# Kernel tuning notes

Measured on AMD Instinct MI355X. Metric: run time of the kernel, lower is better.

The kernel has to match this reference:

```python
import jax, jax.numpy as jnp
import numpy as np

IMG = 800          # image size (square)
STRIDE = 4         # feature-map stride
S = 14             # rcnn_crop_size
C = 256            # crop_channels
N = 512            # number of rpn proposals
NUM_CLASSES = 81   # COCO (incl. background at index 0)
HID = 1024
NMS_TH = 0.5
SCORE_TH = 0.05


def setup_inputs() -> dict:
    key = jax.random.key(0)
    ks = jax.random.split(key, 8)
    features = jax.random.normal(ks[0], (1, C, IMG // STRIDE, IMG // STRIDE), jnp.float32)
    # valid proposal boxes (x0, y0, x1, y1) in image coordinates
    u = jax.random.uniform(ks[1], (N, 4), jnp.float32)
    x0 = u[:, 0] * (IMG - 64.0)
    y0 = u[:, 1] * (IMG - 64.0)
    bw = 16.0 + u[:, 2] * 240.0
    bh = 16.0 + u[:, 3] * 240.0
    proposals = jnp.stack([x0, y0, jnp.minimum(x0 + bw, IMG - 1.0), jnp.minimum(y0 + bh, IMG - 1.0)], axis=1)
    d1 = C * S * S  # 50176
    w1 = jax.random.normal(ks[2], (d1, HID), jnp.float32) * (1.0 / np.sqrt(d1))
    b1 = jnp.zeros((HID,), jnp.float32)
    w2 = jax.random.normal(ks[3], (HID, HID), jnp.float32) * (1.0 / np.sqrt(HID))
    b2 = jnp.zeros((HID,), jnp.float32)
    w_cls = jax.random.normal(ks[4], (HID, NUM_CLASSES), jnp.float32) * (1.0 / np.sqrt(HID))
    b_cls = jnp.zeros((NUM_CLASSES,), jnp.float32)
    w_reg = jax.random.normal(ks[5], (HID, NUM_CLASSES * 4), jnp.float32) * (1.0 / np.sqrt(HID))
    b_reg = jnp.zeros((NUM_CLASSES * 4,), jnp.float32)
    return dict(features=features, proposals=proposals, w1=w1, b1=b1, w2=w2, b2=b2,
                w_cls=w_cls, b_cls=b_cls, w_reg=w_reg, b_reg=b_reg)


def roi_align(feat, boxes):
    """feat: [C,H,W]; boxes: [N,4] image coords -> crops [N,C,S,S] via bilinear sampling (1 sample per bin)."""
    _, H, W = feat.shape
    b = boxes / STRIDE
    t = (jnp.arange(S, dtype=feat.dtype) + 0.5) / S                # [S] bin centers
    xs = b[:, 0:1] + (b[:, 2:3] - b[:, 0:1]) * t                   # [N,S]
    ys = b[:, 1:2] + (b[:, 3:4] - b[:, 1:2]) * t                   # [N,S]
    xx = jnp.broadcast_to(xs[:, None, :], (boxes.shape[0], S, S))  # [N,S,S]
    yy = jnp.broadcast_to(ys[:, :, None], (boxes.shape[0], S, S))
    x0f = jnp.floor(xx); y0f = jnp.floor(yy)
    fx = xx - x0f; fy = yy - y0f
    x0i = jnp.clip(x0f.astype(jnp.int32), 0, W - 1); x1i = jnp.clip(x0i + 1, 0, W - 1)
    y0i = jnp.clip(y0f.astype(jnp.int32), 0, H - 1); y1i = jnp.clip(y0i + 1, 0, H - 1)
    # gathers -> [C,N,S,S]
    v = (((1 - fx) * (1 - fy))[None] * feat[:, y0i, x0i]
         + (fx * (1 - fy))[None] * feat[:, y0i, x1i]
         + ((1 - fx) * fy)[None] * feat[:, y1i, x0i]
         + (fx * fy)[None] * feat[:, y1i, x1i])
    return v.transpose(1, 0, 2, 3)  # [N,C,S,S]


def decode_boxes(rois, d):
    w = rois[:, 2] - rois[:, 0]; h = rois[:, 3] - rois[:, 1]
    cx = rois[:, 0] + 0.5 * w; cy = rois[:, 1] + 0.5 * h
    px = cx + d[:, 0] * w; py = cy + d[:, 1] * h
    pw = w * jnp.exp(jnp.clip(d[:, 2], -4.0, 4.0))
    ph = h * jnp.exp(jnp.clip(d[:, 3], -4.0, 4.0))
    b = jnp.stack([px - 0.5 * pw, py - 0.5 * ph, px + 0.5 * pw, py + 0.5 * ph], axis=1)
    return jnp.clip(b, 0.0, IMG - 1.0)


def iou_matrix(b):
    area = jnp.maximum(b[:, 2] - b[:, 0], 0.0) * jnp.maximum(b[:, 3] - b[:, 1], 0.0)
    ix0 = jnp.maximum(b[:, None, 0], b[None, :, 0])
    iy0 = jnp.maximum(b[:, None, 1], b[None, :, 1])
    ix1 = jnp.minimum(b[:, None, 2], b[None, :, 2])
    iy1 = jnp.minimum(b[:, None, 3], b[None, :, 3])
    inter = jnp.maximum(ix1 - ix0, 0.0) * jnp.maximum(iy1 - iy0, 0.0)
    return inter / (area[:, None] + area[None, :] - inter + 1e-6)


def reference(features, proposals, w1, b1, w2, b2, w_cls, b_cls, w_reg, b_reg):
    # 1) RoIAlign crop
    crops = roi_align(features[0], proposals)              # [N,C,S,S]
    # 2) RCNN head
    x = crops.reshape(N, -1)
    x = jax.nn.relu(x @ w1 + b1)
    x = jax.nn.relu(x @ w2 + b2)
    logits = x @ w_cls + b_cls                             # [N,81]
    deltas = (x @ w_reg + b_reg).reshape(N, NUM_CLASSES, 4)
    # 3) NMS post-processing
    probs = jax.nn.softmax(logits, axis=-1)
    fg = probs[:, 1:]                                      # exclude background
    labels = jnp.argmax(fg, axis=-1) + 1                   # [N]
    scores = jnp.max(fg, axis=-1)                          # [N]
    d = deltas[jnp.arange(N), labels]                      # per-ROI delta of predicted class
    boxes = decode_boxes(proposals, d)
    order = jnp.argsort(-scores)
    bs = boxes[order]; ss = scores[order]; ls = labels[order]
    valid = ss > SCORE_TH
    M = iou_matrix(bs)                                     # [N,N]
    idx = jnp.arange(N)
    def body(i, keep):
        alive = keep[i] & valid[i]
        supp = (M[i] > NMS_TH) & (idx > i) & alive
        return keep & (~supp)
    keep = jax.lax.fori_loop(0, N, body, valid)
    keepf = jax.lax.stop_gradient(keep.astype(bs.dtype))
    final = jnp.concatenate([bs, ss[:, None]], axis=1) * keepf[:, None]   # [N,5]
    return final, ls.astype(jnp.int32), keep
```

## Files before the change

kernel.cpp:

```cpp
#include <hip/hip_runtime.h>
#include <cstdint>

#define F_H 200
#define F_W 200
#define D1  50176
#define NBOX 512
#define NHID 1024

typedef _Float16 f16;
typedef _Float16 half8 __attribute__((ext_vector_type(8)));
typedef _Float16 half4v __attribute__((ext_vector_type(4)));
typedef _Float16 half2v __attribute__((ext_vector_type(2)));
typedef float    f32x4 __attribute__((ext_vector_type(4)));

__device__ __forceinline__ void gload16(const void* g, void* l) {
  __builtin_amdgcn_global_load_lds((const __attribute__((address_space(1))) void*)g,
                                   (__attribute__((address_space(3))) void*)l,
                                   16, 0, 0);
}

__device__ __forceinline__ half2v pkrtz(float a, float b) {
  return __builtin_bit_cast(half2v, __builtin_amdgcn_cvt_pkrtz(a, b));
}

__device__ __forceinline__ void splitf16(float v, f16& h, f16& l) {
  f16 hh = (f16)v;
  float hf = (float)hh;
  if (fabsf(hf) < 6.1035156e-5f) hf = 0.f;
  h = (f16)hh;
  if (fabsf(hf) < 6.1035156e-5f) h = (f16)0.f;
  l = (f16)((v - hf) * 2048.f);
}

__global__ __launch_bounds__(256) void k_roi(const float* __restrict__ feat,
                                             const float* __restrict__ prop,
                                             f16* __restrict__ xhi, f16* __restrict__ xlo) {
  uint32_t idx = blockIdx.x * 256u + threadIdx.x;
  uint32_t n = idx / 25088u;
  uint32_t rem = idx % 25088u;
  uint32_t c = rem / 98u;
  uint32_t r2 = rem % 98u;
  uint32_t i = r2 / 7u;
  uint32_t jp = r2 % 7u;
  float b0 = prop[n * 4 + 0] * 0.25f, b1 = prop[n * 4 + 1] * 0.25f;
  float b2 = prop[n * 4 + 2] * 0.25f, b3 = prop[n * 4 + 3] * 0.25f;
  float ty = ((float)i + 0.5f) * (1.0f / 14.0f);
  float yy = b1 + (b3 - b1) * ty;
  float y0f = floorf(yy);
  float fy = yy - y0f;
  int y0 = (int)y0f; y0 = y0 < 0 ? 0 : (y0 > F_H - 1 ? F_H - 1 : y0);
  int y1 = y0 + 1 > F_H - 1 ? F_H - 1 : y0 + 1;
  const float* fr0 = feat + (size_t)c * (F_H * F_W) + (size_t)y0 * F_W;
  const float* fr1 = feat + (size_t)c * (F_H * F_W) + (size_t)y1 * F_W;
  f16 hs[2], ls[2];
#pragma unroll
  for (int e = 0; e < 2; ++e) {
    uint32_t j = jp * 2u + (uint32_t)e;
    float tx = ((float)j + 0.5f) * (1.0f / 14.0f);
    float xx = b0 + (b2 - b0) * tx;
    float x0f = floorf(xx);
    float fx = xx - x0f;
    int x0 = (int)x0f; x0 = x0 < 0 ? 0 : (x0 > F_W - 1 ? F_W - 1 : x0);
    int x1 = x0 + 1 > F_W - 1 ? F_W - 1 : x0 + 1;
    float v00 = fr0[x0], v01 = fr0[x1], v10 = fr1[x0], v11 = fr1[x1];
    float v = (1.f - fx) * (1.f - fy) * v00 + fx * (1.f - fy) * v01 +
              (1.f - fx) * fy * v10 + fx * fy * v11;
    splitf16(v, hs[e], ls[e]);
  }
  uint32_t base = n * 50176u + c * 196u + i * 14u + jp * 2u;
  half2v hv; hv[0] = hs[0]; hv[1] = hs[1];
  half2v lv; lv[0] = ls[0]; lv[1] = ls[1];
  *(half2v*)(xhi + base) = hv;
  *(half2v*)(xlo + base) = lv;
}

__global__ __launch_bounds__(256) void k_tsplit(const float* __restrict__ W,
                                                f16* __restrict__ hiT, f16* __restrict__ loT,
                                                int Kdim, int Ndim) {
  __shared__ f16 lh[64 * 72];
  __shared__ f16 ll[64 * 72];
  int t = threadIdx.x;
  int k0 = blockIdx.x * 64, n0 = blockIdx.y * 64;
  int r = t >> 2, cq = t & 3;
  const float* src = W + (size_t)(k0 + r) * Ndim + n0 + cq * 16;
  f16 hv[16], lv[16];
#pragma unroll
  for (int e = 0; e < 4; ++e) {
    f32x4 v = *(const f32x4*)(src + e * 4);
#pragma unroll
    for (int x = 0; x < 4; ++x) splitf16(v[x], hv[e * 4 + x], lv[e * 4 + x]);
  }
#pragma unroll
  for (int j = 0; j < 16; ++j) {
    int n_l = cq * 16 + j;
    lh[n_l * 72 + r] = hv[j];
    ll[n_l * 72 + r] = lv[j];
  }
  __syncthreads();
  f16* oh = hiT + (size_t)(n0 + r) * Kdim + k0 + cq * 16;
  f16* ol = loT + (size_t)(n0 + r) * Kdim + k0 + cq * 16;
  *(half8*)(oh)     = *(const half8*)(&lh[r * 72 + cq * 16]);
  *(half8*)(oh + 8) = *(const half8*)(&lh[r * 72 + cq * 16 + 8]);
  *(half8*)(ol)     = *(const half8*)(&ll[r * 72 + cq * 16]);
  *(half8*)(ol + 8) = *(const half8*)(&ll[r * 72 + cq * 16 + 8]);
}

__global__ __launch_bounds__(256) void k_packT(const float* __restrict__ wc_, const float* __restrict__ bc,
                                               const float* __restrict__ wr_, const float* __restrict__ br,
                                               f16* __restrict__ whT_hi, f16* __restrict__ whT_lo,
                                               float* __restrict__ bh) {
  uint32_t idx = blockIdx.x * 256u + threadIdx.x;
  if (idx < 512u * 1024u) {
    uint32_t n = idx >> 10, k = idx & 1023u;
    float v = 0.f;
    if (n < 81u) v = wc_[k * 81u + n];
    else if (n < 405u) v = wr_[k * 324u + (n - 81u)];
    f16 h, l; splitf16(v, h, l);
    whT_hi[idx] = h; whT_lo[idx] = l;
  } else if (idx < 512u * 1024u + 512u) {
    uint32_t n = idx - 512u * 1024u;
    float v = 0.f;
    if (n < 81u) v = bc[n];
    else if (n < 405u) v = br[n - 81u];
    bh[n] = v;
  }
}

__global__ __launch_bounds__(512, 2) void k_gemm2(
    const f16* __restrict__ Ahi, const f16* __restrict__ Alo,
    const f16* __restrict__ Bhi, const f16* __restrict__ Blo,
    float* __restrict__ Cp, int K, int N, int Kc, int nMt, int nNt)
{
  __shared__ char sm[131072];
  const int t = threadIdx.x;
  const int lane = t & 63;
  const int wid = t >> 6;
  const int wr = wid >> 2;
  const int wc = wid & 3;
  const int rl = lane & 15;
  const int lq = lane >> 4;

  int bid = blockIdx.x;
  int low = bid & 7, qq = bid >> 3;
  int nt = qq % nNt;
  int chi = qq / nNt;
  int c = chi * 8 + low;
  int ks = c / nMt;
  int mt = c % nMt;
  const int brow = mt * 256;
  const int nbase = nt * 256;
  const int k0 = ks * Kc;
  const int nk = Kc >> 5;

  uint32_t aoffg[2], aldso[2];
#pragma unroll
  for (int i = 0; i < 2; ++i) {
    uint32_t idx = (uint32_t)t + 512u * i;
    uint32_t q2 = idx >> 2, s = idx & 3;
    uint32_t qh = q2 >> 6;
    uint32_t grh = (qh == 1u) ? 2u : (qh == 2u) ? 1u : qh;
    uint32_t gr = grh * 64u + (q2 & 63u);
    aoffg[i] = (uint32_t)(brow + gr) * (uint32_t)K + (s ^ ((q2 >> 1) & 3u)) * 8u;
    aldso[i] = idx * 16u;
  }
  uint32_t boffg[2], bldso[2];
#pragma unroll
  for (int i = 0; i < 2; ++i) {
    uint32_t idx = (uint32_t)t + 512u * i;
    uint32_t rB = idx >> 2, s = idx & 3;
    boffg[i] = (uint32_t)(nbase + rB) * (uint32_t)K + (s ^ ((rB >> 1) & 3u)) * 8u;
    bldso[i] = idx * 16u;
  }

  const uint32_t swzk = (uint32_t)(lq ^ ((rl >> 1) & 3)) * 16u;
  const uint32_t a_off_lane = (uint32_t)(rl * 64) + swzk;
  const uint32_t b_off_lane = (uint32_t)((wc * 16 + rl) * 64) + swzk;

  f32x4 zero4 = {0.f, 0.f, 0.f, 0.f};
  f32x4 acc[8][4];
#pragma unroll
  for (int m = 0; m < 8; ++m)
#pragma unroll
    for (int n = 0; n < 4; ++n) acc[m][n] = zero4;

#define PH0STAGE(LB, KB) do { \
    gload16(Bhi + boffg[0] + (KB), (LB) + 32768 + bldso[0]); \
    gload16(Blo + boffg[0] + (KB), (LB) + 49152 + bldso[0]); \
    gload16(Bhi + boffg[1] + (KB), (LB) + 32768 + bldso[1]); \
    gload16(Blo + boffg[1] + (KB), (LB) + 49152 + bldso[1]); \
    gload16(Ahi + aoffg[0] + (KB), (LB) + aldso[0]); \
    gload16(Alo + aoffg[0] + (KB), (LB) + 16384 + aldso[0]); \
  } while (0)

#define PH1STAGE(LB, KB) do { \
    gload16(Ahi + aoffg[1] + (KB), (LB) + aldso[1]); \
    gload16(Alo + aoffg[1] + (KB), (LB) + 16384 + aldso[1]); \
  } while (0)

#define COMPUTE_PHASE(P) do { \
    half8 bh2[4], bl2[4]; \
    _Pragma("unroll") \
    for (int nf = 0; nf < 4; ++nf) { \
      bh2[nf] = *(const half8*)(lb + 32768 + nf * 4096 + b_off_lane); \
      bl2[nf] = *(const half8*)(lb + 49152 + nf * 4096 + b_off_lane); \
    } \
    __builtin_amdgcn_s_setprio(1); \
    _Pragma("unroll") \
    for (int mm = 0; mm < 4; ++mm) { \
      const char* ab = lb + (P) * 8192 + wr * 4096 + mm * 1024 + a_off_lane; \
      half8 ah = *(const half8*)(ab); \
      half8 al = *(const half8*)(ab + 16384); \
      _Pragma("unroll") \
      for (int nf = 0; nf < 4; ++nf) { \
        acc[(P)*4+mm][nf] = __builtin_amdgcn_mfma_f32_16x16x32_f16(ah, bh2[nf], acc[(P)*4+mm][nf], 0, 0, 0); \
        f32x4 tt = __builtin_amdgcn_mfma_f32_16x16x32_f16(ah, bl2[nf], zero4, 0, 0, 0); \
        tt = __builtin_amdgcn_mfma_f32_16x16x32_f16(al, bh2[nf], tt, 0, 0, 0); \
        acc[(P)*4+mm][nf] += tt * 4.8828125e-4f; \
      } \
    } \
    __builtin_amdgcn_s_setprio(0); \
  } while (0)

  PH0STAGE(sm, (uint32_t)k0);
  PH1STAGE(sm, (uint32_t)k0);

  int cur = 0;
  for (int kt = 0; kt < nk; ++kt) {
    int ktn = (kt + 1 < nk) ? kt + 1 : kt;
    uint32_t kbn = (uint32_t)(k0 + ktn * 32);
    const char* lb = sm + cur * 65536;
    char* lbn = sm + (cur ^ 1) * 65536;

    asm volatile("s_waitcnt vmcnt(2)" ::: "memory");
    __builtin_amdgcn_s_barrier();
    __builtin_amdgcn_sched_barrier(0);
    PH0STAGE(lbn, kbn);
    COMPUTE_PHASE(0);

    asm volatile("s_waitcnt vmcnt(6)" ::: "memory");
    __builtin_amdgcn_s_barrier();
    __builtin_amdgcn_sched_barrier(0);
    PH1STAGE(lbn, kbn);
    COMPUTE_PHASE(1);

    cur ^= 1;
  }

  float* Cs = Cp + (size_t)ks * ((size_t)512 * (uint32_t)N);
#pragma unroll
  for (int m = 0; m < 8; ++m) {
    int rg = brow + wr * 128 + m * 16 + lq * 4;
#pragma unroll
    for (int nf = 0; nf < 4; ++nf) {
      int cg = nbase + nf * 64 + wc * 16 + rl;
#pragma unroll
      for (int rr = 0; rr < 4; ++rr)
        Cs[(size_t)(rg + rr) * (uint32_t)N + cg] = acc[m][nf][rr];
    }
  }
#undef PH0STAGE
#undef PH1STAGE
}

__global__ __launch_bounds__(512, 2) void k_gemm3(
    const f16* __restrict__ Ahi, const f16* __restrict__ Alo,
    const float* __restrict__ B, float* __restrict__ Cp,
    int K, int N, int Kc, int nMt, int nNt)
{
  __shared__ char sm[131072];
  const int t = threadIdx.x;
  const int lane = t & 63;
  const int wid = t >> 6;
  const int wr = wid >> 2;
  const int wc = wid & 3;
  const int rl = lane & 15;
  const int lq = lane >> 4;

  int bid = blockIdx.x;
  int low = bid & 7, qq = bid >> 3;
  int nt = qq % nNt;
  int chi = qq / nNt;
  int c = chi * 8 + low;
  int ks = c / nMt;
  int mt = c % nMt;
  const int brow = mt * 256;
  const int nbase = nt * 256;
  const int k0 = ks * Kc;
  const int nk = Kc >> 5;

  uint32_t aoffg[2], aldso[2];
#pragma unroll
  for (int i = 0; i < 2; ++i) {
    uint32_t idx = (uint32_t)t + 512u * i;
    uint32_t q2 = idx >> 2, s = idx & 3;
    uint32_t qh = q2 >> 6;
    uint32_t grh = (qh == 1u) ? 2u : (qh == 2u) ? 1u : qh;
    uint32_t gr = grh * 64u + (q2 & 63u);
    aoffg[i] = (uint32_t)(brow + gr) * (uint32_t)K + (s ^ ((q2 >> 1) & 3u)) * 8u;
    aldso[i] = idx * 16u;
  }

  const uint32_t nrow = (uint32_t)t & 255u;
  const uint32_t kh = (uint32_t)t >> 8;
  const float* bsrc0 = B + (size_t)((uint32_t)k0 + kh * 16u) * (uint32_t)N + (uint32_t)nbase + nrow;
  const uint32_t bswz = (nrow >> 1) & 3u;
  const uint32_t wb0 = nrow * 64u + (((kh * 2u)      ^ bswz) << 4);
  const uint32_t wb1 = nrow * 64u + (((kh * 2u + 1u) ^ bswz) << 4);

  const uint32_t swzk = (uint32_t)(lq ^ ((rl >> 1) & 3)) * 16u;
  const uint32_t a_off_lane = (uint32_t)(rl * 64) + swzk;
  const uint32_t b_off_lane = (uint32_t)((wc * 16 + rl) * 64) + swzk;

  f32x4 zero4 = {0.f, 0.f, 0.f, 0.f};
  f32x4 acc[8][4];
#pragma unroll
  for (int m = 0; m < 8; ++m)
#pragma unroll
    for (int n = 0; n < 4; ++n) acc[m][n] = zero4;

  float bx[16], by[16];

#define LOADB(ARR, KT) do { \
    const float* bp = bsrc0 + (size_t)((uint32_t)(KT) * 32u) * (uint32_t)N; \
    _Pragma("unroll") \
    for (int j = 0; j < 16; ++j) ARR[j] = bp[(size_t)j * (uint32_t)N]; \
  } while (0)

#define WRITEB(LB, ARR) do { \
    half8 h0, l0, h1, l1; \
    _Pragma("unroll") \
    for (int j = 0; j < 16; j += 2) { \
      float v0 = ARR[j], v1 = ARR[j + 1]; \
      half2v hp = pkrtz(v0, v1); \
      f16 e0 = (fabsf(v0) >= 6.1035156e-5f) ? hp[0] : (f16)0; \
      f16 e1 = (fabsf(v1) >= 6.1035156e-5f) ? hp[1] : (f16)0; \
      half2v lp = pkrtz((v0 - (float)e0) * 2048.f, (v1 - (float)e1) * 2048.f); \
      if (j < 8) { h0[j] = e0; h0[j + 1] = e1; l0[j] = lp[0]; l0[j + 1] = lp[1]; } \
      else { h1[j - 8] = e0; h1[j - 7] = e1; l1[j - 8] = lp[0]; l1[j - 7] = lp[1]; } \
    } \
    *(half8*)((LB) + 32768 + wb0) = h0; \
    *(half8*)((LB) + 49152 + wb0) = l0; \
    *(half8*)((LB) + 32768 + wb1) = h1; \
    *(half8*)((LB) + 49152 + wb1) = l1; \
  } while (0)

#define STAGE_A4(LB, KB) do { \
    gload16(Ahi + aoffg[0] + (KB), (LB) + aldso[0]); \
    gload16(Alo + aoffg[0] + (KB), (LB) + 16384 + aldso[0]); \
    gload16(Ahi + aoffg[1] + (KB), (LB) + aldso[1]); \
    gload16(Alo + aoffg[1] + (KB), (LB) + 16384 + aldso[1]); \
  } while (0)

#define ITER(KT, IN, OUT) do { \
    int kA = ((KT) + 1 < nk) ? (KT) + 1 : nk - 1; \
    int kB = ((KT) + 2 < nk) ? (KT) + 2 : nk - 1; \
    const char* lb = sm + cur * 65536; \
    char* lbn = sm + (cur ^ 1) * 65536; \
    STAGE_A4(lbn, (uint32_t)(k0 + kA * 32));   \
    LOADB(OUT, kB);                            \
    COMPUTE_PHASE(0); \
    asm volatile("s_waitcnt vmcnt(20)" ::: "memory");   \
    __builtin_amdgcn_sched_barrier(0); \
    WRITEB(lbn, IN); \
    COMPUTE_PHASE(1); \
    asm volatile("s_waitcnt vmcnt(16) lgkmcnt(0)" ::: "memory");   \
    __builtin_amdgcn_sched_barrier(0); \
    __builtin_amdgcn_s_barrier(); \
    cur ^= 1; \
  } while (0)

  LOADB(bx, 0);
  STAGE_A4(sm, (uint32_t)k0);
  asm volatile("s_waitcnt vmcnt(4)" ::: "memory");
  __builtin_amdgcn_sched_barrier(0);
  WRITEB(sm, bx);
  LOADB(by, (nk > 1) ? 1 : 0);
  asm volatile("s_waitcnt vmcnt(16) lgkmcnt(0)" ::: "memory");
  __builtin_amdgcn_sched_barrier(0);
  __builtin_amdgcn_s_barrier();

  int cur = 0;
  int kt = 0;
  for (; kt + 1 < nk; kt += 2) {
    ITER(kt, by, bx);
    ITER(kt + 1, bx, by);
  }
  if (kt < nk) ITER(kt, by, bx);

  float* Cs = Cp + (size_t)ks * ((size_t)512 * (uint32_t)N);
#pragma unroll
  for (int m = 0; m < 8; ++m) {
    int rg = brow + wr * 128 + m * 16 + lq * 4;
#pragma unroll
    for (int nf = 0; nf < 4; ++nf) {
      int cg = nbase + nf * 64 + wc * 16 + rl;
#pragma unroll
      for (int rr = 0; rr < 4; ++rr)
        Cs[(size_t)(rg + rr) * (uint32_t)N + cg] = acc[m][nf][rr];
    }
  }
#undef LOADB
#undef WRITEB
#undef STAGE_A4
#undef ITER
#undef COMPUTE_PHASE
}

__global__ __launch_bounds__(256) void k_reduce(
    const float* __restrict__ parts, const float* __restrict__ bias,
    int nS, int MN4, int Ncols, int relu,
    float* __restrict__ outf, f16* __restrict__ ohi, f16* __restrict__ olo)
{
  uint32_t idx = blockIdx.x * 256u + threadIdx.x;
  if (idx >= (uint32_t)MN4) return;
  f32x4 s = *(const f32x4*)(bias + ((idx * 4u) % (uint32_t)Ncols));
  const f32x4* p4 = (const f32x4*)parts;
  for (int i = 0; i < nS; ++i) s += p4[(size_t)i * (uint32_t)MN4 + idx];
  if (relu) {
#pragma unroll
    for (int j = 0; j < 4; ++j) s[j] = fmaxf(s[j], 0.f);
  }
  if (outf) *(f32x4*)(outf + (size_t)idx * 4) = s;
  if (ohi) {
    half4v h, l;
#pragma unroll
    for (int j = 0; j < 4; ++j) { f16 hh, ll; splitf16(s[j], hh, ll); h[j] = hh; l[j] = ll; }
    *(half4v*)(ohi + (size_t)idx * 4) = h;
    *(half4v*)(olo + (size_t)idx * 4) = l;
  }
}

__global__ __launch_bounds__(256) void k_post(
    const float* __restrict__ ld, const float* __restrict__ prop,
    float* __restrict__ boxes, float* __restrict__ scores, int* __restrict__ labels)
{
  int n = blockIdx.x * 256 + threadIdx.x;
  if (n >= NBOX) return;
  const float* L = ld + (size_t)n * 512;
  float m = L[0];
  for (int j = 1; j < 81; ++j) m = fmaxf(m, L[j]);
  float sum = 0.f;
  for (int j = 0; j < 81; ++j) sum += expf(L[j] - m);
  float best = -1.f; int bj = 1;
  for (int j = 1; j < 81; ++j) {
    float p = expf(L[j] - m) / sum;
    if (p > best) { best = p; bj = j; }
  }
  float d0 = L[81 + bj * 4 + 0];
  float d1 = L[81 + bj * 4 + 1];
  float d2 = L[81 + bj * 4 + 2];
  float d3 = L[81 + bj * 4 + 3];
  float p0 = prop[n * 4 + 0], p1 = prop[n * 4 + 1], p2 = prop[n * 4 + 2], p3 = prop[n * 4 + 3];
  float w = p2 - p0, h = p3 - p1;
  float cx = p0 + 0.5f * w, cy = p1 + 0.5f * h;
  float px = cx + d0 * w, py = cy + d1 * h;
  float pw = w * expf(fminf(fmaxf(d2, -4.f), 4.f));
  float ph = h * expf(fminf(fmaxf(d3, -4.f), 4.f));
  float bx0 = px - 0.5f * pw, by0 = py - 0.5f * ph;
  float bx1 = px + 0.5f * pw, by1 = py + 0.5f * ph;
  boxes[n * 4 + 0] = fminf(fmaxf(bx0, 0.f), 799.f);
  boxes[n * 4 + 1] = fminf(fmaxf(by0, 0.f), 799.f);
  boxes[n * 4 + 2] = fminf(fmaxf(bx1, 0.f), 799.f);
  boxes[n * 4 + 3] = fminf(fmaxf(by1, 0.f), 799.f);
  scores[n] = best;
  labels[n] = bj;
}

__global__ __launch_bounds__(512) void k_sort(
    const float* __restrict__ scores, const float* __restrict__ boxes, const int* __restrict__ labels,
    float* __restrict__ bs, float* __restrict__ ss, int* __restrict__ ls)
{
  __shared__ unsigned long long keys[512];
  int t = threadIdx.x;
  unsigned sb = __float_as_uint(scores[t]);
  keys[t] = ((unsigned long long)(0xFFFFFFFFu - sb) << 32) | (unsigned)t;
  __syncthreads();
  for (int k = 2; k <= 512; k <<= 1) {
    for (int j = k >> 1; j > 0; j >>= 1) {
      int p = t ^ j;
      if (p > t) {
        unsigned long long a = keys[t], b = keys[p];
        bool asc = ((t & k) == 0);
        if (asc ? (a > b) : (a < b)) { keys[t] = b; keys[p] = a; }
      }
      __syncthreads();
    }
  }
  unsigned o = (unsigned)(keys[t] & 0xFFFFFFFFu);
  ss[t] = scores[o];
  ls[t] = labels[o];
  bs[t * 4 + 0] = boxes[o * 4 + 0];
  bs[t * 4 + 1] = boxes[o * 4 + 1];
  bs[t * 4 + 2] = boxes[o * 4 + 2];
  bs[t * 4 + 3] = boxes[o * 4 + 3];
}

__global__ __launch_bounds__(64) void k_mask(const float* __restrict__ bs,
                                             unsigned long long* __restrict__ mask) {
  int i = blockIdx.x;
  int lane = threadIdx.x;
  float ax0 = bs[i * 4], ay0 = bs[i * 4 + 1], ax1 = bs[i * 4 + 2], ay1 = bs[i * 4 + 3];
  float aarea = fmaxf(ax1 - ax0, 0.f) * fmaxf(ay1 - ay0, 0.f);
  for (int w = 0; w < 8; ++w) {
    int j = w * 64 + lane;
    float bx0 = bs[j * 4], by0 = bs[j * 4 + 1], bx1 = bs[j * 4 + 2], by1 = bs[j * 4 + 3];
    float barea = fmaxf(bx1 - bx0, 0.f) * fmaxf(by1 - by0, 0.f);
    float ix0 = fmaxf(ax0, bx0), iy0 = fmaxf(ay0, by0);
    float ix1 = fminf(ax1, bx1), iy1 = fminf(ay1, by1);
    float inter = fmaxf(ix1 - ix0, 0.f) * fmaxf(iy1 - iy0, 0.f);
    float iou = inter / (aarea + barea - inter + 1e-6f);
    bool cond = (iou > 0.5f) && (j > i);
    unsigned long long b = __ballot(cond);
    if (lane == 0) mask[i * 8 + w] = b;
  }
}

__global__ __launch_bounds__(64) void k_nms(const unsigned long long* __restrict__ mask,
                                            const float* __restrict__ ss,
                                            const float* __restrict__ bs,
                                            const int* __restrict__ ls,
                                            float* __restrict__ out) {
  int lane = threadIdx.x;
  unsigned long long bal[8];
  for (int w = 0; w < 8; ++w) bal[w] = __ballot(ss[w * 64 + lane] > 0.05f);
  unsigned long long keep = (lane < 8) ? bal[lane] : 0ULL;
  for (int i = 0; i < 512; ++i) {
    unsigned long long kw = __shfl(keep, i >> 6);
    if ((kw >> (i & 63)) & 1ULL) {
      unsigned long long mi = (lane < 8) ? mask[i * 8 + lane] : 0ULL;
      keep &= ~mi;
    }
  }
  __shared__ unsigned long long kws[8];
  if (lane < 8) kws[lane] = keep;
  __syncthreads();
  for (int it = 0; it < 56; ++it) {
    int idx = lane + it * 64;
    float val;
    if (idx < 2560) {
      int i = idx / 5, c2 = idx % 5;
      bool kb = (kws[i >> 6] >> (i & 63)) & 1ULL;
      val = kb ? (c2 < 4 ? bs[i * 4 + c2] : ss[i]) : 0.f;
    } else if (idx < 3072) {
      int i = idx - 2560;
      val = (float)ls[i];
    } else {
      int i = idx - 3072;
      val = ((kws[i >> 6] >> (i & 63)) & 1ULL) ? 1.f : 0.f;
    }
    out[idx] = val;
  }
}

static constexpr size_t SZ_X    = (size_t)NBOX * D1 * 2;
static constexpr size_t SZ_PART = (size_t)32 * 512 * 1024 * 4;
static constexpr size_t SZ_H    = (size_t)512 * 1024 * 2;
static constexpr size_t NP_XHI   = 0;
static constexpr size_t NP_XLO   = NP_XHI + SZ_X;
static constexpr size_t NP_PART  = NP_XLO + SZ_X;
static constexpr size_t NP_W2HIT = NP_PART + SZ_PART;
static constexpr size_t NP_W2LOT = NP_W2HIT + (size_t)1024 * 1024 * 2;
static constexpr size_t NP_WHHIT = NP_W2LOT + (size_t)1024 * 1024 * 2;
static constexpr size_t NP_WHLOT = NP_WHHIT + (size_t)512 * 1024 * 2;
static constexpr size_t NP_BH    = NP_WHLOT + (size_t)512 * 1024 * 2;
static constexpr size_t NP_H1HI  = NP_BH + 4096;
static constexpr size_t NP_H1LO  = NP_H1HI + SZ_H;
static constexpr size_t NP_H2HI  = NP_H1LO + SZ_H;
static constexpr size_t NP_H2LO  = NP_H2HI + SZ_H;
static constexpr size_t NP_LD    = NP_H2LO + SZ_H;
static constexpr size_t NP_BOX   = NP_LD + (size_t)512 * 512 * 4;
static constexpr size_t NP_SC    = NP_BOX + 512 * 4 * 4;
static constexpr size_t NP_LB    = NP_SC + 4096;
static constexpr size_t NP_BS    = NP_LB + 4096;
static constexpr size_t NP_SS    = NP_BS + 512 * 4 * 4;
static constexpr size_t NP_LS    = NP_SS + 4096;
static constexpr size_t NP_MASK  = NP_LS + 4096;
static constexpr size_t NP_END   = NP_MASK + (size_t)512 * 8 * 8;

extern "C" void kernel_launch(void* const* d_in, const int* in_sizes, int n_in,
                              void* d_out, int out_size, void* d_ws, size_t ws_size,
                              hipStream_t stream)
{
  (void)in_sizes; (void)n_in;
  const float* feat = (const float*)d_in[0];
  const float* prop = (const float*)d_in[1];
  const float* w1   = (const float*)d_in[2];
  const float* b1   = (const float*)d_in[3];
  const float* w2   = (const float*)d_in[4];
  const float* b2   = (const float*)d_in[5];
  const float* wcls = (const float*)d_in[6];
  const float* bcls = (const float*)d_in[7];
  const float* wreg = (const float*)d_in[8];
  const float* breg = (const float*)d_in[9];
  float* out = (float*)d_out;
  char* W = (char*)d_ws;

  if (ws_size < NP_END) {
    (void)hipMemsetAsync(out, 0x7f, (size_t)out_size * 4, stream);
    return;
  }

  f16*   xhi   = (f16*)(W + NP_XHI);
  f16*   xlo   = (f16*)(W + NP_XLO);
  float* parts = (float*)(W + NP_PART);
  f16*   w2hiT = (f16*)(W + NP_W2HIT);
  f16*   w2loT = (f16*)(W + NP_W2LOT);
  f16*   whHiT = (f16*)(W + NP_WHHIT);
  f16*   whLoT = (f16*)(W + NP_WHLOT);
  float* bhead = (float*)(W + NP_BH);
  f16*   h1hi  = (f16*)(W + NP_H1HI);
  f16*   h1lo  = (f16*)(W + NP_H1LO);
  f16*   h2hi  = (f16*)(W + NP_H2HI);
  f16*   h2lo  = (f16*)(W + NP_H2LO);
  float* ldbuf = (float*)(W + NP_LD);
  float* boxes = (float*)(W + NP_BOX);
  float* scores= (float*)(W + NP_SC);
  int*   labels= (int*)(W + NP_LB);
  float* bsrt  = (float*)(W + NP_BS);
  float* ssrt  = (float*)(W + NP_SS);
  int*   lsrt  = (int*)(W + NP_LS);
  unsigned long long* maskb = (unsigned long long*)(W + NP_MASK);

  k_roi<<<50176, 256, 0, stream>>>(feat, prop, xhi, xlo);
  k_tsplit<<<dim3(1024 / 64, 1024 / 64), 256, 0, stream>>>(w2, w2hiT, w2loT, 1024, 1024);
  k_packT<<<2050, 256, 0, stream>>>(wcls, bcls, wreg, breg, whHiT, whLoT, bhead);

  k_gemm3<<<256, 512, 0, stream>>>(xhi, xlo, w1, parts, D1, 1024, 1568, 2, 4);
  k_reduce<<<512, 256, 0, stream>>>(parts, b1, 32, 131072, 1024, 1, nullptr, h1hi, h1lo);

  k_gemm2<<<256, 512, 0, stream>>>(h1hi, h1lo, w2hiT, w2loT, parts, 1024, 1024, 32, 2, 4);
  k_reduce<<<512, 256, 0, stream>>>(parts, b2, 32, 131072, 1024, 1, nullptr, h2hi, h2lo);

  k_gemm2<<<128, 512, 0, stream>>>(h2hi, h2lo, whHiT, whLoT, parts, 1024, 512, 32, 2, 2);
  k_reduce<<<256, 256, 0, stream>>>(parts, bhead, 32, 65536, 512, 0, ldbuf, nullptr, nullptr);

  k_post<<<2, 256, 0, stream>>>(ldbuf, prop, boxes, scores, labels);
  k_sort<<<1, 512, 0, stream>>>(scores, boxes, labels, bsrt, ssrt, lsrt);
  k_mask<<<512, 64, 0, stream>>>(bsrt, maskb);
  k_nms<<<1, 64, 0, stream>>>(maskb, ssrt, bsrt, lsrt, out);
}
```

Before: 429.3 us.

## Warp-specialize first-layer GEMM with dedicated producer waves for loads

The first large GEMM kernel grows from 512 to 768 threads. Four extra producer waves now issue all A-tile global-to-LDS loads, load the fp32 B rows, and write the hi/lo fp16 split into shared memory. The eight consumer waves only run the MFMA compute phases and store results. The intent is to move load latency and conversion work off the compute waves and overlap them more fully. In exchange, occupancy drops to one block per CU and producer threads carry 64 registers of B data.

```diff
diff --git a/kernel.cpp b/kernel.cpp
--- a/kernel.cpp
+++ b/kernel.cpp
@@ -262,7 +262,7 @@
 #undef PH1STAGE
 }
 
-__global__ __launch_bounds__(512, 2) void k_gemm3(
+__global__ __launch_bounds__(768, 1) void k_gemm3(
     const f16* __restrict__ Ahi, const f16* __restrict__ Alo,
     const float* __restrict__ B, float* __restrict__ Cp,
     int K, int N, int Kc, int nMt, int nNt)
@@ -271,7 +271,8 @@
   const int t = threadIdx.x;
   const int lane = t & 63;
   const int wid = t >> 6;
-  const int wr = wid >> 2;
+  const bool isProd = (t >= 512);
+  const int wr = (wid >> 2) & 1;
   const int wc = wid & 3;
   const int rl = lane & 15;
   const int lq = lane >> 4;
@@ -288,10 +289,11 @@
   const int k0 = ks * Kc;
   const int nk = Kc >> 5;
 
-  uint32_t aoffg[2], aldso[2];
-#pragma unroll
-  for (int i = 0; i < 2; ++i) {
-    uint32_t idx = (uint32_t)t + 512u * i;
+  const int tp = t & 255;
+  uint32_t aoffg[4], aldso[4];
+#pragma unroll
+  for (int i = 0; i < 4; ++i) {
+    uint32_t idx = (uint32_t)tp + 256u * i;
     uint32_t q2 = idx >> 2, s = idx & 3;
     uint32_t qh = q2 >> 6;
     uint32_t grh = (qh == 1u) ? 2u : (qh == 2u) ? 1u : qh;
@@ -299,13 +301,12 @@
     aoffg[i] = (uint32_t)(brow + gr) * (uint32_t)K + (s ^ ((q2 >> 1) & 3u)) * 8u;
     aldso[i] = idx * 16u;
   }
-
-  const uint32_t nrow = (uint32_t)t & 255u;
-  const uint32_t kh = (uint32_t)t >> 8;
-  const float* bsrc0 = B + (size_t)((uint32_t)k0 + kh * 16u) * (uint32_t)N + (uint32_t)nbase + nrow;
-  const uint32_t bswz = (nrow >> 1) & 3u;
-  const uint32_t wb0 = nrow * 64u + (((kh * 2u)      ^ bswz) << 4);
-  const uint32_t wb1 = nrow * 64u + (((kh * 2u + 1u) ^ bswz) << 4);
+  const float* bsrc0 = B + (size_t)(uint32_t)k0 * (uint32_t)N + (uint32_t)nbase + (uint32_t)tp;
+  const uint32_t bswz = ((uint32_t)tp >> 1) & 3u;
+  uint32_t wbseg[4];
+#pragma unroll
+  for (int s2 = 0; s2 < 4; ++s2)
+    wbseg[s2] = (uint32_t)tp * 64u + ((((uint32_t)s2) ^ bswz) << 4);
 
   const uint32_t swzk = (uint32_t)(lq ^ ((rl >> 1) & 3)) * 16u;
   const uint32_t a_off_lane = (uint32_t)(rl * 64) + swzk;
@@ -318,37 +319,62 @@
 #pragma unroll
     for (int n = 0; n < 4; ++n) acc[m][n] = zero4;
 
-  float bx[16], by[16];
+  float bxr[32], byr[32];
 
 #define LOADB(ARR, KT) do { \
-    const float* bp = bsrc0 + (size_t)((uint32_t)(KT) * 32u) * (uint32_t)N; \
     _Pragma("unroll") \
-    for (int j = 0; j < 16; ++j) ARR[j] = bp[(size_t)j * (uint32_t)N]; \
+    for (int j = 0; j < 32; ++j) \
+      ARR[j] = bsrc0[(size_t)((uint32_t)(KT) * 32u + (uint32_t)j) * (uint32_t)N]; \
   } while (0)
 
 #define WRITEB(LB, ARR) do { \
-    half8 h0, l0, h1, l1; \
     _Pragma("unroll") \
-    for (int j = 0; j < 16; j += 2) { \
-      float v0 = ARR[j], v1 = ARR[j + 1]; \
-      half2v hp = pkrtz(v0, v1); \
-      f16 e0 = (fabsf(v0) >= 6.1035156e-5f) ? hp[0] : (f16)0; \
-      f16 e1 = (fabsf(v1) >= 6.1035156e-5f) ? hp[1] : (f16)0; \
-      half2v lp = pkrtz((v0 - (float)e0) * 2048.f, (v1 - (float)e1) * 2048.f); \
-      if (j < 8) { h0[j] = e0; h0[j + 1] = e1; l0[j] = lp[0]; l0[j + 1] = lp[1]; } \
-      else { h1[j - 8] = e0; h1[j - 7] = e1; l1[j - 8] = lp[0]; l1[j - 7] = lp[1]; } \
+    for (int s2 = 0; s2 < 4; ++s2) { \
+      half8 h8, l8; \
+      _Pragma("unroll") \
+      for (int j = 0; j < 8; j += 2) { \
+        float v0 = ARR[s2 * 8 + j], v1 = ARR[s2 * 8 + j + 1]; \
+        half2v hp = pkrtz(v0, v1); \
+        f16 e0 = (fabsf(v0) >= 6.1035156e-5f) ? hp[0] : (f16)0; \
+        f16 e1 = (fabsf(v1) >= 6.1035156e-5f) ? hp[1] : (f16)0; \
+        half2v lp = pkrtz((v0 - (float)e0) * 2048.f, (v1 - (float)e1) * 2048.f); \
+        h8[j] = e0; h8[j + 1] = e1; l8[j] = lp[0]; l8[j + 1] = lp[1]; \
+      } \
+      *(half8*)((LB) + 32768 + wbseg[s2]) = h8; \
+      *(half8*)((LB) + 49152 + wbseg[s2]) = l8; \
     } \
-    *(half8*)((LB) + 32768 + wb0) = h0; \
-    *(half8*)((LB) + 49152 + wb0) = l0; \
-    *(half8*)((LB) + 32768 + wb1) = h1; \
-    *(half8*)((LB) + 49152 + wb1) = l1; \
-  } while (0)
-
-#define STAGE_A4(LB, KB) do { \
-    gload16(Ahi + aoffg[0] + (KB), (LB) + aldso[0]); \
-    gload16(Alo + aoffg[0] + (KB), (LB) + 16384 + aldso[0]); \
-    gload16(Ahi + aoffg[1] + (KB), (LB) + aldso[1]); \
-    gload16(Alo + aoffg[1] + (KB), (LB) + 16384 + aldso[1]); \
+  } while (0)
+
+#define STAGE_A8(LB, KB) do { \
+    _Pragma("unroll") \
+    for (int i = 0; i < 4; ++i) { \
+      gload16(Ahi + aoffg[i] + (KB), (LB) + aldso[i]); \
+      gload16(Alo + aoffg[i] + (KB), (LB) + 16384 + aldso[i]); \
+    } \
+  } while (0)
+
+#define COMPUTE_PHASE(P) do { \
+    half8 bh2[4], bl2[4]; \
+    _Pragma("unroll") \
+    for (int nf = 0; nf < 4; ++nf) { \
+      bh2[nf] = *(const half8*)(lb + 32768 + nf * 4096 + b_off_lane); \
+      bl2[nf] = *(const half8*)(lb + 49152 + nf * 4096 + b_off_lane); \
+    } \
+    __builtin_amdgcn_s_setprio(1); \
+    _Pragma("unroll") \
+    for (int mm = 0; mm < 4; ++mm) { \
+      const char* ab = lb + (P) * 8192 + wr * 4096 + mm * 1024 + a_off_lane; \
+      half8 ah = *(const half8*)(ab); \
+      half8 al = *(const half8*)(ab + 16384); \
+      _Pragma("unroll") \
+      for (int nf = 0; nf < 4; ++nf) { \
+        acc[(P)*4+mm][nf] = __builtin_amdgcn_mfma_f32_16x16x32_f16(ah, bh2[nf], acc[(P)*4+mm][nf], 0, 0, 0); \
+        f32x4 tt = __builtin_amdgcn_mfma_f32_16x16x32_f16(ah, bl2[nf], zero4, 0, 0, 0); \
+        tt = __builtin_amdgcn_mfma_f32_16x16x32_f16(al, bh2[nf], tt, 0, 0, 0); \
+        acc[(P)*4+mm][nf] += tt * 4.8828125e-4f; \
+      } \
+    } \
+    __builtin_amdgcn_s_setprio(0); \
   } while (0)
 
 #define ITER(KT, IN, OUT) do { \
@@ -356,52 +382,61 @@
     int kB = ((KT) + 2 < nk) ? (KT) + 2 : nk - 1; \
     const char* lb = sm + cur * 65536; \
     char* lbn = sm + (cur ^ 1) * 65536; \
-    STAGE_A4(lbn, (uint32_t)(k0 + kA * 32));   \
-    LOADB(OUT, kB);                            \
-    COMPUTE_PHASE(0); \
-    asm volatile("s_waitcnt vmcnt(20)" ::: "memory");   \
-    __builtin_amdgcn_sched_barrier(0); \
-    WRITEB(lbn, IN); \
-    COMPUTE_PHASE(1); \
-    asm volatile("s_waitcnt vmcnt(16) lgkmcnt(0)" ::: "memory");   \
-    __builtin_amdgcn_sched_barrier(0); \
+    if (isProd) { \
+      STAGE_A8(lbn, (uint32_t)(k0 + kA * 32));             \
+      asm volatile("s_waitcnt vmcnt(8)" ::: "memory");     \
+      __builtin_amdgcn_sched_barrier(0); \
+      WRITEB(lbn, IN); \
+      LOADB(OUT, kB);                                      \
+      asm volatile("s_waitcnt vmcnt(32) lgkmcnt(0)" ::: "memory");   \
+      __builtin_amdgcn_sched_barrier(0); \
+    } else { \
+      COMPUTE_PHASE(0); \
+      COMPUTE_PHASE(1); \
+      asm volatile("s_waitcnt lgkmcnt(0)" ::: "memory"); \
+      __builtin_amdgcn_sched_barrier(0); \
+    } \
     __builtin_amdgcn_s_barrier(); \
     cur ^= 1; \
   } while (0)
 
-  LOADB(bx, 0);
-  STAGE_A4(sm, (uint32_t)k0);
-  asm volatile("s_waitcnt vmcnt(4)" ::: "memory");
-  __builtin_amdgcn_sched_barrier(0);
-  WRITEB(sm, bx);
-  LOADB(by, (nk > 1) ? 1 : 0);
-  asm volatile("s_waitcnt vmcnt(16) lgkmcnt(0)" ::: "memory");
-  __builtin_amdgcn_sched_barrier(0);
+  if (isProd) {
+    LOADB(bxr, 0);
+    STAGE_A8(sm, (uint32_t)k0);
+    asm volatile("s_waitcnt vmcnt(8)" ::: "memory");
+    __builtin_amdgcn_sched_barrier(0);
+    WRITEB(sm, bxr);
+    LOADB(byr, (nk > 1) ? 1 : 0);
+    asm volatile("s_waitcnt vmcnt(32) lgkmcnt(0)" ::: "memory");
+    __builtin_amdgcn_sched_barrier(0);
+  }
   __builtin_amdgcn_s_barrier();
 
   int cur = 0;
   int kt = 0;
   for (; kt + 1 < nk; kt += 2) {
-    ITER(kt, by, bx);
-    ITER(kt + 1, bx, by);
-  }
-  if (kt < nk) ITER(kt, by, bx);
-
-  float* Cs = Cp + (size_t)ks * ((size_t)512 * (uint32_t)N);
-#pragma unroll
-  for (int m = 0; m < 8; ++m) {
-    int rg = brow + wr * 128 + m * 16 + lq * 4;
-#pragma unroll
-    for (int nf = 0; nf < 4; ++nf) {
-      int cg = nbase + nf * 64 + wc * 16 + rl;
-#pragma unroll
-      for (int rr = 0; rr < 4; ++rr)
-        Cs[(size_t)(rg + rr) * (uint32_t)N + cg] = acc[m][nf][rr];
+    ITER(kt, byr, bxr);
+    ITER(kt + 1, bxr, byr);
+  }
+  if (kt < nk) ITER(kt, byr, bxr);
+
+  if (!isProd) {
+    float* Cs = Cp + (size_t)ks * ((size_t)512 * (uint32_t)N);
+#pragma unroll
+    for (int m = 0; m < 8; ++m) {
+      int rg = brow + wr * 128 + m * 16 + lq * 4;
+#pragma unroll
+      for (int nf = 0; nf < 4; ++nf) {
+        int cg = nbase + nf * 64 + wc * 16 + rl;
+#pragma unroll
+        for (int rr = 0; rr < 4; ++rr)
+          Cs[(size_t)(rg + rr) * (uint32_t)N + cg] = acc[m][nf][rr];
+      }
     }
   }
 #undef LOADB
 #undef WRITEB
-#undef STAGE_A4
+#undef STAGE_A8
 #undef ITER
 #undef COMPUTE_PHASE
 }
@@ -625,7 +660,7 @@
   k_tsplit<<<dim3(1024 / 64, 1024 / 64), 256, 0, stream>>>(w2, w2hiT, w2loT, 1024, 1024);
   k_packT<<<2050, 256, 0, stream>>>(wcls, bcls, wreg, breg, whHiT, whLoT, bhead);
 
-  k_gemm3<<<256, 512, 0, stream>>>(xhi, xlo, w1, parts, D1, 1024, 1568, 2, 4);
+  k_gemm3<<<256, 768, 0, stream>>>(xhi, xlo, w1, parts, D1, 1024, 1568, 2, 4);
   k_reduce<<<512, 256, 0, stream>>>(parts, b1, 32, 131072, 1024, 1, nullptr, h1hi, h1lo);
 
   k_gemm2<<<256, 512, 0, stream>>>(h1hi, h1lo, w2hiT, w2loT, parts, 1024, 1024, 32, 2, 4);
```

Result: slower. 1.320 ms (+207.5%).
